# Optimization experiments

Measured on AMD Instinct MI355X. Metric: run time of the kernel, lower is better.

## Reference

```python
import jax, jax.numpy as jnp
import numpy as np

B0, K, H, W = 8, 1, 512, 512
S, CS, NMS, M = 25, 51, 5, 2048
REG_W, COV_POW = 1.0, 0.5

def _gauss_kernel(n):
    x = jnp.linspace(-1.0, 1.0, n)
    g = jnp.exp(-x * x / 0.5)
    return g / g.sum()

def _conv1d2d(x, k1d, horizontal, pad_h, pad_w):
    # x: [B,1,H,W]; replicates torch F.conv2d with the given (possibly asymmetric) padding
    kern = k1d.reshape(1, 1, 1, -1) if horizontal else k1d.reshape(1, 1, -1, 1)
    return jax.lax.conv_general_dilated(x, kern, (1, 1), [(pad_h, pad_h), (pad_w, pad_w)],
                                        dimension_numbers=("NCHW", "OIHW", "NCHW"))

def bilinear_sample(img, pts):
    # img [B,C,H,W], pts [B,N,2] (x,y in [-1,1]); grid_sample bilinear, align_corners=False, zero padding
    Bb, C, Hh, Ww = img.shape
    x = (pts[..., 0] + 1.0) * 0.5 * Ww - 0.5
    y = (pts[..., 1] + 1.0) * 0.5 * Hh - 0.5
    x0 = jnp.floor(x); y0 = jnp.floor(y)
    wx = x - x0; wy = y - y0
    x0i = x0.astype(jnp.int32); y0i = y0.astype(jnp.int32)
    flat = img.reshape(Bb, C, Hh * Ww)
    def tap(yi, xi, w):
        ok = ((yi >= 0) & (yi < Hh) & (xi >= 0) & (xi < Ww)).astype(img.dtype)
        idx = jnp.clip(yi, 0, Hh - 1) * Ww + jnp.clip(xi, 0, Ww - 1)  # [B,N]
        v = jnp.take_along_axis(flat, idx[:, None, :], axis=2)        # [B,C,N]
        return v * (w * ok)[:, None, :]
    return (tap(y0i, x0i, (1 - wy) * (1 - wx)) + tap(y0i, x0i + 1, (1 - wy) * wx)
            + tap(y0i + 1, x0i, wy * (1 - wx)) + tap(y0i + 1, x0i + 1, wy * wx))

def compute_matchability(keypoint_p, has_depth, Bt):
    G = _gauss_kernel(S)
    # NOTE: faithful to original asymmetric padding bug: pad H while convolving along W, then pad W while convolving along H
    s = _conv1d2d(keypoint_p.reshape(Bt, 1, H, W), G, True, S // 2, 0)
    s = _conv1d2d(s, G, False, 0, S // 2)
    log_p_hat = jax.nn.log_softmax(jnp.log(s.reshape(Bt, H * W) + 1e-8), axis=-1)
    sd = _conv1d2d(has_depth.reshape(Bt, 1, H, W), G, True, 0, S // 2)
    sd = _conv1d2d(sd, G, False, S // 2, 0).reshape(Bt, H * W)
    p = sd / sd.sum(-1, keepdims=True)
    return jnp.sum(jnp.where(p > 0, p * (jnp.log(jnp.maximum(p, 1e-30)) - log_p_hat), 0.0), axis=-1)

def sample_keypoints(sm):
    # sm [B,H,W]; coverage-reweighted NMS + top-k (topk=True, subpixel=False)
    wcov = jnp.exp(-jnp.square(jnp.linspace(-2.0, 2.0, CS)))
    ld = _conv1d2d(((sm + 1e-6) * 1e4)[:, None], wcov, True, 0, CS // 2)
    ld = _conv1d2d(ld, wcov, False, CS // 2, 0)[:, 0]
    sm = sm * (ld + 1e-8) ** (-COV_POW)
    p = NMS // 2
    mx = jax.lax.reduce_window(sm, -jnp.inf, jax.lax.max, (1, NMS, NMS), (1, 1, 1),
                               [(0, 0), (p, p), (p, p)])
    sm = sm * (sm == mx)
    _, inds = jax.lax.top_k(sm.reshape(-1, H * W), M)
    xs = (jnp.arange(W) + 0.5) * 2.0 / W - 1.0
    ys = (jnp.arange(H) + 0.5) * 2.0 / H - 1.0
    grid = jnp.stack(jnp.meshgrid(xs, ys, indexing="xy"), axis=-1).reshape(H * W, 2)
    return jnp.take(grid, inds, axis=0)  # [B,M,2] normalized (x,y)

def masked_log_softmax(logits, mask):
    return jax.nn.log_softmax(jnp.where(mask, logits, -1e9), axis=-1)

def _reward(d):
    return jnp.exp(-100.0 * d)

def _forward(scoremap, gt_warp_A2B, gt_warp_B2A, valid_A2B, valid_B2A, has_depth):
    sg = jax.lax.stop_gradient
    lA = scoremap[:B0].reshape(B0, K, H * W)
    lB = scoremap[B0:].reshape(B0, K, H * W)
    logits = jnp.concatenate([lA, lB], 0)                                   # [2B,K,HW]
    kp_p = jax.nn.softmax(logits.reshape(2 * B0, K * H * W), -1).reshape(2 * B0, K, H * W).sum(1)
    match_loss = compute_matchability(kp_p, sg(has_depth), 2 * B0).mean()
    # sparse branch is under torch.set_grad_enabled(False)
    kpts_A = sample_keypoints(sg(kp_p[:B0]).reshape(B0, H, W))
    kpts_B = sample_keypoints(sg(kp_p[B0:]).reshape(B0, H, W))
    kpts_A2B = bilinear_sample(sg(gt_warp_A2B[..., 2:]).transpose(0, 3, 1, 2), kpts_A).transpose(0, 2, 1)
    kpts_B2A = bilinear_sample(sg(gt_warp_B2A[..., 2:]).transpose(0, 3, 1, 2), kpts_B).transpose(0, 2, 1)
    legit_A2B = bilinear_sample(sg(valid_A2B)[:, None], kpts_A)[:, 0] > 0   # [B,M]
    legit_B2A = bilinear_sample(sg(valid_B2A)[:, None], kpts_B)[:, 0] > 0
    dA = jnp.sqrt(jnp.sum(jnp.square(kpts_A2B[:, :, None] - kpts_B[:, None]), -1) + 1e-12).min(-1)
    dB = jnp.sqrt(jnp.sum(jnp.square(kpts_B2A[:, :, None] - kpts_A[:, None]), -1) + 1e-12).min(-1)
    rA = _reward(dA); rB = _reward(dB)
    slA = bilinear_sample(lA.reshape(B0, 1, H, W), kpts_A)[:, 0]            # [B,M]
    slB = bilinear_sample(lB.reshape(B0, 1, H, W), kpts_B)[:, 0]
    lpA = masked_log_softmax(slA, legit_A2B)
    lpB = masked_log_softmax(slB, legit_B2A)
    sparse = -jnp.sum(jnp.where(legit_A2B, rA * lpA, 0.0)) - jnp.sum(jnp.where(legit_B2A, rB * lpB, 0.0))
    return sparse + REG_W * match_loss

def setup_inputs() -> dict:
    key = jax.random.key(0)
    ks = jax.random.split(key, 6)
    scoremap = jax.random.normal(ks[0], (2 * B0, K, H, W), jnp.float32)
    gt_warp_A2B = jax.random.uniform(ks[1], (B0, H, W, 4), jnp.float32, -1.0, 1.0)
    gt_warp_B2A = jax.random.uniform(ks[2], (B0, H, W, 4), jnp.float32, -1.0, 1.0)
    valid_A2B = (jax.random.uniform(ks[3], (B0, H, W)) > 0.3).astype(jnp.float32)
    valid_B2A = (jax.random.uniform(ks[4], (B0, H, W)) > 0.3).astype(jnp.float32)
    has_depth = (jax.random.uniform(ks[5], (2 * B0, H, W)) > 0.3).astype(jnp.float32)
    return dict(scoremap=scoremap, gt_warp_A2B=gt_warp_A2B, gt_warp_B2A=gt_warp_B2A,
                valid_A2B=valid_A2B, valid_B2A=valid_B2A, has_depth=has_depth)

def reference(scoremap, gt_warp_A2B, gt_warp_B2A, valid_A2B, valid_B2A, has_depth):
    return _forward(scoremap, gt_warp_A2B, gt_warp_B2A, valid_A2B, valid_B2A, has_depth)
```

## Files before the change

### kernel.cpp

```cpp
#include <hip/hip_runtime.h>

#define HH 512
#define WW 512
#define HW_ 262144
#define NIMG 16
#define MK 2048
#define CAPB 4096
#define SCAP 32768
#define SBUFN 768

static constexpr size_t OFF_B1    = 16777216;
static constexpr size_t OFF_SMALL = 50331648;
static constexpr size_t OFF_SEL  = 4194304;
static constexpr size_t OFF_BND  = 4325376;
static constexpr size_t OFF_PP   = 4849664;
static constexpr size_t OFF_WXp  = 5111808;
static constexpr size_t OFF_WYp  = 5242880;
static constexpr size_t OFF_LG   = 5373952;
static constexpr size_t OFF_SL   = 5505024;
static constexpr size_t OFF_PMIN = 5636096;
static constexpr size_t OFF_HIST = 33554432;
static constexpr size_t OFF_SURV = 33554432 + 4194304;

#define CSTRIDE 32

__device__ __forceinline__ float wred64(float v) {
  for (int m = 1; m < 64; m <<= 1) v += __shfl_xor(v, m);
  return v;
}

__device__ __forceinline__ void g25_wave0(float* g) {
  int t = threadIdx.x;
  if (t < 64) {
    float raw = 0.0f;
    if (t < 25) {
      float x = -1.0f + (float)t * (2.0f / 24.0f);
      raw = expf(-(x * x) / 0.5f);
    }
    float s = raw;
    for (int m = 1; m < 64; m <<= 1) s += __shfl_xor(s, m);
    if (t < 25) g[t] = raw / s;
  }
}
__device__ __forceinline__ void w51_wave0(float* wc) {
  int t = threadIdx.x;
  if (t < 51) {
    float x = -2.0f + (float)t * (4.0f / 50.0f);
    wc[t] = expf(-x * x);
  }
}

template<int B>
__device__ __forceinline__ float brsum(float v, float* red) {
  int t = threadIdx.x;
  red[t] = v; __syncthreads();
  for (int s = B >> 1; s > 0; s >>= 1) {
    if (t < s) red[t] += red[t + s];
    __syncthreads();
  }
  float r = red[0]; __syncthreads();
  return r;
}
template<int B>
__device__ __forceinline__ float brmax(float v, float* red) {
  int t = threadIdx.x;
  red[t] = v; __syncthreads();
  for (int s = B >> 1; s > 0; s >>= 1) {
    if (t < s) red[t] = fmaxf(red[t], red[t + s]);
    __syncthreads();
  }
  float r = red[0]; __syncthreads();
  return r;
}

__global__ void __launch_bounds__(256)
k_pre(const float* __restrict__ x, const float* __restrict__ hd, float* A,
      float* sume, float* sumS, float* Zb) {
  __shared__ float g[25];
  __shared__ float gp[26];
  __shared__ float red[12];
  int tid = threadIdx.x;
  g25_wave0(g);
  if (tid == 0) {
    float c = 0.0f;
    gp[0] = 0.0f;
    for (int k = 0; k < 25; k++) { c += g[k]; gp[k + 1] = c; }
  }
  size_t base = (size_t)blockIdx.x * 1024;
  size_t e = base + tid * 4;
  float4 xs = *(const float4*)(x + e);
  float4 hs = *(const float4*)(hd + e);
  __syncthreads();
  int rem = (int)(e & (HW_ - 1));
  int y = rem >> 9, x0 = rem & 511;
  float wv;
  {
    int k0 = y - 499; if (k0 < 0) k0 = 0;
    int k1 = y + 12;  if (k1 > 24) k1 = 24;
    wv = gp[k1 + 1] - gp[k0];
  }
  float cwv[4], cpv[4];
#pragma unroll
  for (int q = 0; q < 4; q++) {
    int i = x0 + q;
    int lo = i - 487; if (lo < 0) lo = 0;
    int hi = i;       if (hi > 24) hi = 24;
    cwv[q] = gp[hi + 1] - gp[lo];
    int lo2 = i - 499; if (lo2 < 0) lo2 = 0;
    int hi2 = i + 12;  if (hi2 > 24) hi2 = 24;
    cpv[q] = gp[hi2 + 1] - gp[lo2];
  }
  float e0 = expf(xs.x), e1 = expf(xs.y), e2 = expf(xs.z), e3 = expf(xs.w);
  *(float4*)(A + e) = make_float4(e0, e1, e2, e3);
  float r0 = (e0 + e1) + (e2 + e3);
  float r1 = (e0 * cwv[0] + e1 * cwv[1] + e2 * cwv[2] + e3 * cwv[3]) * wv;
  float r2 = (hs.x * cpv[0] + hs.y * cpv[1] + hs.z * cpv[2] + hs.w * cpv[3]) * wv;
  r0 = wred64(r0); r1 = wred64(r1); r2 = wred64(r2);
  int wid = tid >> 6;
  if ((tid & 63) == 0) { red[wid] = r0; red[4 + wid] = r1; red[8 + wid] = r2; }
  __syncthreads();
  if (tid == 0) {
    int img = (int)(base >> 18);
    atomicAdd(&sume[img * CSTRIDE], red[0] + red[1] + red[2] + red[3]);
    atomicAdd(&sumS[img * CSTRIDE], red[4] + red[5] + red[6] + red[7]);
    atomicAdd(&Zb[img * CSTRIDE], red[8] + red[9] + red[10] + red[11]);
  }
}

__global__ void __launch_bounds__(256)
k_hconv(const float* __restrict__ A, const float* __restrict__ hd,
        const float* __restrict__ sume, float* b12) {
  __shared__ __align__(16) float ta[512];
  __shared__ __align__(16) float th[536];
  __shared__ float g[25];
  int tid = threadIdx.x;
  int blk = blockIdx.x;
  int img = blk >> 9;
  size_t rowoff = (size_t)blk * 512;
  g25_wave0(g);
  ((float2*)ta)[tid] = *(const float2*)(A + rowoff + tid * 2);
  ((float2*)(th + 12))[tid] = *(const float2*)(hd + rowoff + tid * 2);
  if (tid < 12) { th[tid] = 0.0f; th[524 + tid] = 0.0f; }
  __syncthreads();
  float inv = 1.0f / sume[img * CSTRIDE];
  int j = 2 * tid;
  float v1a = 0.0f, v1b = 0.0f;
  if (tid >= 6 && tid <= 249) {
    float w[26];
#pragma unroll
    for (int d = 0; d < 26; d++) w[d] = ta[j - 12 + d];
#pragma unroll
    for (int d = 0; d < 25; d++) {
      v1a = fmaf(g[d], w[d], v1a);
      v1b = fmaf(g[d], w[d + 1], v1b);
    }
  }
  float v2a = 0.0f, v2b = 0.0f;
  {
    float u[26];
#pragma unroll
    for (int d = 0; d < 26; d++) u[d] = th[j + d];
#pragma unroll
    for (int d = 0; d < 25; d++) {
      v2a = fmaf(g[d], u[d], v2a);
      v2b = fmaf(g[d], u[d + 1], v2b);
    }
  }
  *(float4*)(b12 + (rowoff + j) * 2) =
      make_float4(v1a * inv, v2a, v1b * inv, v2b);
}

__global__ void __launch_bounds__(256)
k_match(const float* __restrict__ b12,
        const float* __restrict__ sume, const float* sumS, const float* Zb,
        float* macc) {
  __shared__ float g[25];
  __shared__ __align__(16) float t12[88 * 128];
  __shared__ float red4[4];
  g25_wave0(g);
  int blk = blockIdx.x;
  int img = blk >> 6;
  int ty = (blk >> 3) & 7;
  int tx = blk & 7;
  int y0 = ty * 64, x0 = tx * 64;
  const float* base12 = b12 + (size_t)img * HW_ * 2;
  for (int i = threadIdx.x; i < 88 * 32; i += 256) {
    int r = i >> 5, c4 = i & 31;
    int y = y0 + r - 12;
    float4 v = make_float4(0.f, 0.f, 0.f, 0.f);
    if (y >= 0 && y < 512) {
      size_t px = (size_t)y * 512 + x0 + c4 * 2;
      v = *(const float4*)(base12 + px * 2);
    }
    *(float4*)(t12 + r * 128 + c4 * 4) = v;
  }
  __syncthreads();
  float Z = Zb[img * CSTRIDE];
  float inv = 1.0f / sume[img * CSTRIDE];
  float logS = logf(sumS[img * CSTRIDE] * inv + (float)HW_ * 1e-8f);
  float acc = 0.0f;
  for (int w = threadIdx.x; w < 1024; w += 256) {
    int rg = w >> 6, c = w & 63;
    int r0 = rg * 4;
    float s[4] = {0.f, 0.f, 0.f, 0.f};
    float d[4] = {0.f, 0.f, 0.f, 0.f};
#pragma unroll
    for (int i = 0; i < 28; i++) {
      float2 v = *(const float2*)(t12 + (r0 + i) * 128 + c * 2);
#pragma unroll
      for (int jj = 0; jj < 4; jj++) {
        if (i >= jj && i - jj < 25) {
          s[jj] = fmaf(g[i - jj], v.x, s[jj]);
          d[jj] = fmaf(g[i - jj], v.y, d[jj]);
        }
      }
    }
#pragma unroll
    for (int jj = 0; jj < 4; jj++) {
      float p = d[jj] / Z;
      if (p > 0.0f)
        acc += p * (logf(fmaxf(p, 1e-30f)) - (logf(s[jj] + 1e-8f) - logS));
    }
  }
  acc = wred64(acc);
  if ((threadIdx.x & 63) == 0) red4[threadIdx.x >> 6] = acc;
  __syncthreads();
  if (threadIdx.x == 0)
    atomicAdd(macc, red4[0] + red4[1] + red4[2] + red4[3]);
}

__global__ void __launch_bounds__(256)
k_h51(const float* __restrict__ A, const float* __restrict__ sume, float* out,
      unsigned* __restrict__ hist) {
  __shared__ float wc[51];
  __shared__ __align__(16) float ta[564];
  int tid = threadIdx.x;
  int blk = blockIdx.x;
  int img = blk >> 9;
  size_t rowoff = (size_t)blk * 512;
  w51_wave0(wc);
  if (tid < 32)
    ((uint4*)hist)[(size_t)blk * 32 + tid] = make_uint4(0u, 0u, 0u, 0u);
  float s1 = 1e4f / sume[img * CSTRIDE];
  for (int i = tid; i < 562; i += 256) {
    int j = i - 25;
    ta[i] = ((unsigned)j < 512u) ? fmaf(A[rowoff + j], s1, 1e-2f) : 0.0f;
  }
  __syncthreads();
  int j = 2 * tid;
  float w[52];
#pragma unroll
  for (int d = 0; d < 52; d++) w[d] = ta[j + d];
  float va = 0.0f, vb = 0.0f;
#pragma unroll
  for (int d = 0; d < 51; d++) {
    va = fmaf(wc[d], w[d], va);
    vb = fmaf(wc[d], w[d + 1], vb);
  }
  ((float2*)out)[blk * 256 + tid] = make_float2(va, vb);
}

__global__ void __launch_bounds__(512, 6)
k_smwnms(const float* __restrict__ A, const float* __restrict__ sume,
         const float* __restrict__ b1,
         unsigned long long* surv, unsigned* scnt, unsigned* hist) {
  __shared__ float wc[53];
  __shared__ __align__(16) float tb1[119 * 68];
  __shared__ __align__(16) float tsm[68 * 68];
  __shared__ unsigned lcnt;
  __shared__ unsigned gbase;
  float* hm = tb1;
  unsigned long long* sbuf = (unsigned long long*)(tb1 + 4352);
  int tid = threadIdx.x;
  w51_wave0(wc);
  if (tid == 51 || tid == 52) wc[tid] = 0.0f;
  if (tid == 0) lcnt = 0;
  int blk = blockIdx.x;
  int img = blk >> 6;
  int ty = (blk >> 3) & 7;
  int tx = blk & 7;
  int y0 = ty * 64, x0 = tx * 64;
  const float* base = b1 + (size_t)img * HW_;
  {
    float2 vreg[8];
    int laddr[8];
#pragma unroll
    for (int k = 0; k < 8; k++) {
      int i = tid + k * 512;
      bool ok = (i < 119 * 34);
      int r = i / 34, c2 = i - r * 34;
      int y = y0 + r - 27;
      int x = x0 + c2 * 2 - 2;
      float2 v = make_float2(0.0f, 0.0f);
      if (ok && (unsigned)y < 512u && (unsigned)x < 512u)
        v = *(const float2*)(base + (size_t)y * 512 + x);
      vreg[k] = v;
      laddr[k] = ok ? (r * 68 + c2 * 2) : -1;
    }
#pragma unroll
    for (int k = 0; k < 8; k++)
      if (laddr[k] >= 0) *(float2*)(tb1 + laddr[k]) = vreg[k];
  }
  __syncthreads();
  float inv = 1.0f / sume[img * CSTRIDE];
  const float* abase = A + (size_t)img * HW_;
  if (tid < 23 * 17) {
    int rg = tid / 17, cg = tid - rg * 17;
    int r0 = rg * 3, c0 = cg * 4;
    int nr = (r0 <= 65) ? 3 : 2;
    float2 apre[3][2];
#pragma unroll
    for (int jj = 0; jj < 3; jj++) {
      int y = y0 + r0 + jj - 2;
      int xb = x0 + c0 - 2;
      apre[jj][0] = make_float2(0.f, 0.f);
      apre[jj][1] = make_float2(0.f, 0.f);
      if ((unsigned)y < 512u) {
        const float* ar = abase + (size_t)y * 512;
        if ((unsigned)xb < 512u) apre[jj][0] = *(const float2*)(ar + xb);
        if ((unsigned)(xb + 2) < 512u) apre[jj][1] = *(const float2*)(ar + xb + 2);
      }
    }
    float a0x = 0.f, a0y = 0.f, a0z = 0.f, a0w = 0.f;
    float a1x = 0.f, a1y = 0.f, a1z = 0.f, a1w = 0.f;
    float a2x = 0.f, a2y = 0.f, a2z = 0.f, a2w = 0.f;
    float w1 = 0.f, w2 = 0.f;
    const float* tp = tb1 + r0 * 68 + c0;
#pragma unroll 4
    for (int i = 0; i < 53; i++) {
      float4 v = *(const float4*)(tp + i * 68);
      float w0 = wc[i];
      a0x = fmaf(w0, v.x, a0x); a0y = fmaf(w0, v.y, a0y);
      a0z = fmaf(w0, v.z, a0z); a0w = fmaf(w0, v.w, a0w);
      a1x = fmaf(w1, v.x, a1x); a1y = fmaf(w1, v.y, a1y);
      a1z = fmaf(w1, v.z, a1z); a1w = fmaf(w1, v.w, a1w);
      a2x = fmaf(w2, v.x, a2x); a2y = fmaf(w2, v.y, a2y);
      a2z = fmaf(w2, v.z, a2z); a2w = fmaf(w2, v.w, a2w);
      w2 = w1; w1 = w0;
    }
    auto storerow = [&](int jj, float ax, float ay, float az, float aw,
                        float2 p0, float2 p1) {
      int r = r0 + jj;
      int y = y0 + r - 2;
      int xb = x0 + c0 - 2;
      float4 res = make_float4(-3.4e38f, -3.4e38f, -3.4e38f, -3.4e38f);
      if ((unsigned)y < 512u) {
        if ((unsigned)xb < 512u) {
          res.x = (p0.x * inv) / sqrtf(ax + 1e-8f);
          res.y = (p0.y * inv) / sqrtf(ay + 1e-8f);
        }
        if ((unsigned)(xb + 2) < 512u) {
          res.z = (p1.x * inv) / sqrtf(az + 1e-8f);
          res.w = (p1.y * inv) / sqrtf(aw + 1e-8f);
        }
      }
      *(float4*)(tsm + r * 68 + c0) = res;
    };
    storerow(0, a0x, a0y, a0z, a0w, apre[0][0], apre[0][1]);
    storerow(1, a1x, a1y, a1z, a1w, apre[1][0], apre[1][1]);
    if (nr == 3) storerow(2, a2x, a2y, a2z, a2w, apre[2][0], apre[2][1]);
  }
  __syncthreads();
  for (int i = tid; i < 68 * 16; i += 512) {
    int r = i >> 4, cg = i & 15;
    const float* row = tsm + r * 68 + cg * 4;
    float4 v0 = *(const float4*)(row);
    float4 v1 = *(const float4*)(row + 4);
    float p01 = fmaxf(v0.x, v0.y), p12 = fmaxf(v0.y, v0.z);
    float p23 = fmaxf(v0.z, v0.w), p34 = fmaxf(v0.w, v1.x);
    float p45 = fmaxf(v1.x, v1.y), p56 = fmaxf(v1.y, v1.z);
    float m0 = fmaxf(fmaxf(p01, p23), v1.x);
    float m1 = fmaxf(fmaxf(p12, p34), v1.y);
    float m2 = fmaxf(fmaxf(p23, p45), v1.z);
    float m3 = fmaxf(fmaxf(p34, p56), v1.w);
    *(float4*)(hm + r * 64 + cg * 4) = make_float4(m0, m1, m2, m3);
  }
  __syncthreads();
  for (int k0 = 0; k0 < 2; k0++) {
    int i = tid + k0 * 512;
    int r = i >> 4, cb = (i & 15) * 4;
    const float* tp2 = tsm + (r + 2) * 68 + cb + 2;
    float2 va = *(const float2*)(tp2);
    float2 vb = *(const float2*)(tp2 + 2);
    float4 m0 = *(const float4*)(hm + r * 64 + cb);
    float4 m1 = *(const float4*)(hm + (r + 1) * 64 + cb);
    float4 m2 = *(const float4*)(hm + (r + 2) * 64 + cb);
    float4 m3 = *(const float4*)(hm + (r + 3) * 64 + cb);
    float4 m4 = *(const float4*)(hm + (r + 4) * 64 + cb);
    float Mx = fmaxf(fmaxf(m0.x, m1.x), fmaxf(fmaxf(m2.x, m3.x), m4.x));
    float My = fmaxf(fmaxf(m0.y, m1.y), fmaxf(fmaxf(m2.y, m3.y), m4.y));
    float Mz = fmaxf(fmaxf(m0.z, m1.z), fmaxf(fmaxf(m2.z, m3.z), m4.z));
    float Mw = fmaxf(fmaxf(m0.w, m1.w), fmaxf(fmaxf(m2.w, m3.w), m4.w));
    auto keepf = [&](float vk, float Mk, int k) {
      if (vk == Mk && vk != 0.0f) {
        unsigned p = atomicAdd(&lcnt, 1u);
        unsigned bits = __float_as_uint(vk);
        unsigned idx = (unsigned)((y0 + r) * 512 + x0 + cb + k);
        if (p < SBUFN)
          sbuf[p] = ((unsigned long long)bits << 32) |
                    (unsigned long long)(idx ^ 0xFFFFFFFFu);
        atomicAdd(&hist[(size_t)img * 65536 + (bits >> 16)], 1u);
      }
    };
    keepf(va.x, Mx, 0); keepf(va.y, My, 1);
    keepf(vb.x, Mz, 2); keepf(vb.y, Mw, 3);
  }
  __syncthreads();
  unsigned total = lcnt; if (total > SBUFN) total = SBUFN;
  if (tid == 0) gbase = atomicAdd(&scnt[img * CSTRIDE], total);
  __syncthreads();
  unsigned gb = gbase;
  for (unsigned i = tid; i < total; i += 512) {
    unsigned p = gb + i;
    if (p < SCAP) surv[(size_t)img * SCAP + p] = sbuf[i];
  }
}

__global__ void __launch_bounds__(1024)
k_thresh(const unsigned* __restrict__ hist, unsigned* Tb, unsigned* needb) {
  int img = blockIdx.x;
  const unsigned* h = hist + (size_t)img * 65536;
  __shared__ unsigned wsum[16];
  __shared__ unsigned wpre[16];
  int t = threadIdx.x;
  int b0 = 65472 - 64 * t;
  const uint4* hv = (const uint4*)(h + b0);
  unsigned s = 0;
#pragma unroll
  for (int k = 0; k < 16; k++) {
    uint4 u = hv[k];
    s += u.x + u.y + u.z + u.w;
  }
  if (b0 == 0) s += 0x00100000u - h[0];
  unsigned inc = s;
  for (int m = 1; m < 64; m <<= 1) {
    unsigned o = __shfl_up(inc, m);
    if ((t & 63) >= m) inc += o;
  }
  if ((t & 63) == 63) wsum[t >> 6] = inc;
  __syncthreads();
  if (t < 16) {
    unsigned p = 0;
    for (int k = 0; k < 16; k++) if (k < t) p += wsum[k];
    wpre[t] = p;
  }
  __syncthreads();
  unsigned pre = wpre[t >> 6] + inc - s;
  if (pre < MK && pre + s >= MK) {
    unsigned c = pre;
    for (int k = 0; k < 64; k++) {
      int bin = 65535 - (t * 64 + k);
      unsigned cnt = (bin == 0) ? 0x00100000u : h[bin];
      if (c + cnt >= MK) { Tb[img * CSTRIDE] = (unsigned)bin; needb[img * CSTRIDE] = MK - c; break; }
      c += cnt;
    }
  }
}

__global__ void k_collect(const unsigned long long* __restrict__ surv,
                          const unsigned* __restrict__ scnt,
                          const unsigned* __restrict__ Tb,
                          unsigned* selcnt, unsigned* sel,
                          unsigned* bcnt, unsigned long long* bnd) {
  int blk = blockIdx.x;
  int img = blk >> 7;
  int i = (blk & 127) * 256 + threadIdx.x;
  unsigned cnt = scnt[img * CSTRIDE]; if (cnt > SCAP) cnt = SCAP;
  unsigned long long entry = ((unsigned)i < cnt) ? surv[(size_t)img * SCAP + i] : 0ull;
  unsigned bits = (unsigned)(entry >> 32);
  unsigned bin = bits >> 16;
  unsigned T = Tb[img * CSTRIDE];
  bool ok = (unsigned)i < cnt;
  bool c1 = ok && (bin > T);
  bool c2 = ok && (bin == T);
  int lane = threadIdx.x & 63;
  unsigned long long lowmask = (1ull << lane) - 1ull;

  unsigned long long m1 = __ballot(c1);
  if (m1) {
    int leader = __ffsll(m1) - 1;
    unsigned base = 0;
    if (lane == leader) base = atomicAdd(&selcnt[img * CSTRIDE], (unsigned)__popcll(m1));
    base = __shfl(base, leader);
    if (c1) {
      unsigned p = base + (unsigned)__popcll(m1 & lowmask);
      if (p < MK) sel[img * MK + p] = (unsigned)(entry & 0xFFFFFFFFull) ^ 0xFFFFFFFFu;
    }
  }
  unsigned long long m2 = __ballot(c2);
  if (m2) {
    int leader = __ffsll(m2) - 1;
    unsigned base = 0;
    if (lane == leader) base = atomicAdd(&bcnt[img * CSTRIDE], (unsigned)__popcll(m2));
    base = __shfl(base, leader);
    if (c2) {
      unsigned p = base + (unsigned)__popcll(m2 & lowmask);
      if (p < CAPB) bnd[(size_t)img * CAPB + p] = entry;
    }
  }
}

__global__ void __launch_bounds__(1024)
k_finsel(const unsigned long long* __restrict__ bnd, const unsigned* bcnt,
         const unsigned* needb, const unsigned* selcnt, unsigned* sel) {
  int img = blockIdx.x;
  __shared__ unsigned long long key[CAPB];
  unsigned bn = bcnt[img * CSTRIDE];
  int n = (bn < CAPB) ? (int)bn : CAPB;
  int np2 = 2;
  while (np2 < n) np2 <<= 1;
  int t = threadIdx.x;
  for (int k = t; k < np2; k += 1024)
    key[k] = (k < n) ? bnd[(size_t)img * CAPB + k] : 0ull;
  __syncthreads();
  for (int sz = 2; sz <= np2; sz <<= 1) {
    for (int st = sz >> 1; st > 0; st >>= 1) {
      for (int i = t; i < np2; i += 1024) {
        int l = i ^ st;
        if (l > i) {
          unsigned long long a = key[i], b = key[l];
          bool up = ((i & sz) == 0);
          if (up ? (a < b) : (a > b)) { key[i] = b; key[l] = a; }
        }
      }
      __syncthreads();
    }
  }
  unsigned c1 = selcnt[img * CSTRIDE]; if (c1 > MK) c1 = MK;
  unsigned need = needb[img * CSTRIDE];
  unsigned kk = need; if (kk > MK - c1) kk = MK - c1;
  for (unsigned m = t; m < MK - c1; m += 1024) {
    unsigned v = 0u;
    if (m < kk && m < (unsigned)n)
      v = (unsigned)(key[m] & 0xFFFFFFFFull) ^ 0xFFFFFFFFu;
    sel[img * MK + c1 + m] = v;
  }
}

__global__ void k_prep(const unsigned* __restrict__ sel, const float* __restrict__ scoremap,
                       const float* __restrict__ gtA, const float* __restrict__ gtB,
                       const float* __restrict__ vA, const float* __restrict__ vB,
                       float2* pp, float* wx, float* wy, float* lg, float* sl) {
  int t = blockIdx.x * 256 + threadIdx.x;
  int img = t >> 11;
  unsigned idx = sel[t] & (HW_ - 1);
  int h = idx >> 9, w = idx & 511;
  pp[t] = make_float2((w + 0.5f) * (2.0f / 512.0f) - 1.0f,
                      (h + 0.5f) * (2.0f / 512.0f) - 1.0f);
  int b = (img < 8) ? img : img - 8;
  const float* gt = (img < 8) ? gtA : gtB;
  const float* vv = (img < 8) ? vA : vB;
  size_t pix = (size_t)b * HW_ + idx;
  float2 gxy = *(const float2*)(gt + pix * 4 + 2);
  wx[t] = gxy.x;
  wy[t] = gxy.y;
  lg[t] = (vv[pix] > 0.0f) ? 1.0f : 0.0f;
  sl[t] = scoremap[(size_t)img * HW_ + idx];
}

__global__ void __launch_bounds__(256)
k_mindist(const float2* __restrict__ pp,
          const float* __restrict__ wx, const float* __restrict__ wy,
          float* pmin) {
  __shared__ float2 opp[512];
  int blk = blockIdx.x;
  int img = blk >> 5;
  int qc = (blk >> 2) & 7;
  int oc = blk & 3;
  const float2* ob = pp + (size_t)(img ^ 8) * MK + oc * 512;
  for (int k = threadIdx.x; k < 512; k += 256) opp[k] = ob[k];
  __syncthreads();
  int m = img * MK + qc * 256 + threadIdx.x;
  float ax = wx[m], ay = wy[m];
  float d[8];
#pragma unroll
  for (int u = 0; u < 8; u++) d[u] = 3.4e38f;
  for (int n = 0; n < 512; n += 8) {
#pragma unroll
    for (int u = 0; u < 8; u++) {
      float2 o = opp[n + u];
      float dx = ax - o.x, dy = ay - o.y;
      d[u] = fminf(d[u], fmaf(dx, dx, dy * dy));
    }
  }
  float d2 = fminf(fminf(fminf(d[0], d[1]), fminf(d[2], d[3])),
                   fminf(fminf(d[4], d[5]), fminf(d[6], d[7])));
  pmin[oc * (NIMG * MK) + m] = d2;
}

__global__ void __launch_bounds__(1024)
k_loss(const float* __restrict__ sl, const float* __restrict__ lg,
       const float* __restrict__ pmin, float* sacc, float* macc, float* out,
       unsigned* ldone) {
  int img = blockIdx.x;
  __shared__ float red[1024];
  int t = threadIdx.x;
  int i0 = img * MK + t, i1 = i0 + 1024;
  float s0 = sl[i0], s1 = sl[i1];
  float g0 = lg[i0], g1 = lg[i1];
  float l0 = (g0 > 0.0f) ? s0 : -1e9f;
  float l1 = (g1 > 0.0f) ? s1 : -1e9f;
  float mx = brmax<1024>(fmaxf(l0, l1), red);
  float se = brsum<1024>(expf(l0 - mx) + expf(l1 - mx), red);
  float lse = mx + logf(se);
  const int ST = NIMG * MK;
  float a = 0.0f;
  if (g0 > 0.0f) {
    float mn = fminf(fminf(pmin[i0], pmin[ST + i0]),
                     fminf(pmin[2 * ST + i0], pmin[3 * ST + i0]));
    float r0 = expf(-100.0f * sqrtf(mn + 1e-12f));
    a += r0 * (s0 - lse);
  }
  if (g1 > 0.0f) {
    float mn = fminf(fminf(pmin[i1], pmin[ST + i1]),
                     fminf(pmin[2 * ST + i1], pmin[3 * ST + i1]));
    float r1 = expf(-100.0f * sqrtf(mn + 1e-12f));
    a += r1 * (s1 - lse);
  }
  float tot = brsum<1024>(a, red);
  if (t == 0) {
    atomicAdd(sacc, -tot);
    __threadfence();
    unsigned dnum = atomicAdd(ldone, 1u);
    if (dnum == NIMG - 1) {
      float sv = atomicAdd(sacc, 0.0f);
      float mv = atomicAdd(macc, 0.0f);
      out[0] = sv + mv * (1.0f / 16.0f);
    }
  }
}

extern "C" void kernel_launch(void* const* d_in, const int* in_sizes, int n_in,
                              void* d_out, int out_size, void* d_ws, size_t ws_size,
                              hipStream_t stream) {
  const float* scoremap = (const float*)d_in[0];
  const float* gtA = (const float*)d_in[1];
  const float* gtB = (const float*)d_in[2];
  const float* vA  = (const float*)d_in[3];
  const float* vB  = (const float*)d_in[4];
  const float* hd  = (const float*)d_in[5];

  char* ws = (char*)d_ws;
  float* A   = (float*)(ws);
  float* B12 = (float*)(ws + OFF_B1);
  float* B1p = (float*)(ws + OFF_B1);

  char* sm = ws + OFF_SMALL;
  float*    sume   = (float*)(sm + 0);
  float*    sumS   = (float*)(sm + 2048);
  float*    Zb     = (float*)(sm + 4096);
  unsigned* Tb     = (unsigned*)(sm + 6144);
  unsigned* needb  = (unsigned*)(sm + 8192);
  unsigned* selcnt = (unsigned*)(sm + 10240);
  unsigned* bcnt   = (unsigned*)(sm + 12288);
  float*    macc   = (float*)(sm + 14336);
  float*    sacc   = (float*)(sm + 14464);
  unsigned* scnt   = (unsigned*)(sm + 16384);
  unsigned* ldone  = (unsigned*)(sm + 20480);

  unsigned* hist = (unsigned*)(ws + OFF_HIST);
  unsigned long long* surv = (unsigned long long*)(ws + OFF_SURV);
  unsigned* sel  = (unsigned*)(ws + OFF_SEL);
  unsigned long long* bnd = (unsigned long long*)(ws + OFF_BND);
  float2* pp = (float2*)(ws + OFF_PP);
  float* wx = (float*)(ws + OFF_WXp);
  float* wy = (float*)(ws + OFF_WYp);
  float* lg = (float*)(ws + OFF_LG);
  float* sl = (float*)(ws + OFF_SL);
  float* pmin = (float*)(ws + OFF_PMIN);

  float* out = (float*)d_out;

  hipMemsetAsync(sm, 0, 32768, stream);

  k_pre<<<4096, 256, 0, stream>>>(scoremap, hd, A, sume, sumS, Zb);

  k_hconv<<<8192, 256, 0, stream>>>(A, hd, sume, B12);
  k_match<<<1024, 256, 0, stream>>>(B12, sume, sumS, Zb, macc);

  k_h51<<<8192, 256, 0, stream>>>(A, sume, B1p, hist);

  k_smwnms<<<1024, 512, 0, stream>>>(A, sume, B1p, surv, scnt, hist);
  k_thresh<<<16, 1024, 0, stream>>>(hist, Tb, needb);
  k_collect<<<2048, 256, 0, stream>>>(surv, scnt, Tb, selcnt, sel, bcnt, bnd);
  k_finsel<<<16, 1024, 0, stream>>>(bnd, bcnt, needb, selcnt, sel);

  k_prep<<<128, 256, 0, stream>>>(sel, scoremap, gtA, gtB, vA, vB, pp, wx, wy, lg, sl);
  k_mindist<<<512, 256, 0, stream>>>(pp, wx, wy, pmin);
  k_loss<<<16, 1024, 0, stream>>>(sl, lg, pmin, sacc, macc, out, ldone);
}
```

Baseline: 288.5 us.

## Stream vertical convolutions from global memory into register sliding windows

Both k_match and k_smwnms stop staging halo tiles in shared memory. Each thread now walks down one column straight from global memory and accumulates 16 or 17 output rows in registers using a shifting weight window. k_smwnms also folds the horizontal and vertical max passes into a single 5x5 pass read from the tsm tile, and its launch bounds go from 6 to 8 blocks. The goal is to cut LDS traffic and footprint and raise occupancy, at the cost of strided uncoalesced-per-thread global loads, higher register pressure, and threads idling on the 68-of-128 column mapping.

After: 660.4 us. 2.29x slower.

```diff
diff --git a/kernel.cpp b/kernel.cpp
--- a/kernel.cpp
+++ b/kernel.cpp
@@ -174,58 +174,57 @@
 k_match(const float* __restrict__ b12,
         const float* __restrict__ sume, const float* sumS, const float* Zb,
         float* macc) {
-  __shared__ float g[25];
-  __shared__ __align__(16) float t12[88 * 128];
+  __shared__ float g[40];
   __shared__ float red4[4];
+  int tid = threadIdx.x;
   g25_wave0(g);
+  if (tid >= 25 && tid < 40) g[tid] = 0.0f;
   int blk = blockIdx.x;
   int img = blk >> 6;
   int ty = (blk >> 3) & 7;
   int tx = blk & 7;
   int y0 = ty * 64, x0 = tx * 64;
   const float* base12 = b12 + (size_t)img * HW_ * 2;
-  for (int i = threadIdx.x; i < 88 * 32; i += 256) {
-    int r = i >> 5, c4 = i & 31;
-    int y = y0 + r - 12;
-    float4 v = make_float4(0.f, 0.f, 0.f, 0.f);
-    if (y >= 0 && y < 512) {
-      size_t px = (size_t)y * 512 + x0 + c4 * 2;
-      v = *(const float4*)(base12 + px * 2);
-    }
-    *(float4*)(t12 + r * 128 + c4 * 4) = v;
-  }
-  __syncthreads();
   float Z = Zb[img * CSTRIDE];
-  float inv = 1.0f / sume[img * CSTRIDE];
-  float logS = logf(sumS[img * CSTRIDE] * inv + (float)HW_ * 1e-8f);
+  float invs = 1.0f / sume[img * CSTRIDE];
+  float logS = logf(sumS[img * CSTRIDE] * invs + (float)HW_ * 1e-8f);
+  __syncthreads();
+  int seg = tid >> 6;
+  int c = tid & 63;
+  int r0 = seg * 16;
+  const float* colp = base12 + (size_t)(x0 + c) * 2;
+  float s[16], d[16], wreg[16];
+#pragma unroll
+  for (int jj = 0; jj < 16; jj++) { s[jj] = 0.f; d[jj] = 0.f; wreg[jj] = 0.f; }
+  int ybase = y0 + r0 - 12;
+#pragma unroll
+  for (int i = 0; i < 40; i++) {
+    int y = ybase + i;
+    float vx = 0.0f, vy = 0.0f;
+    if ((unsigned)y < 512u) {
+      float2 v = *(const float2*)(colp + (size_t)y * 1024);
+      vx = v.x; vy = v.y;
+    }
+#pragma unroll
+    for (int jj = 15; jj >= 1; jj--) wreg[jj] = wreg[jj - 1];
+    wreg[0] = g[i];
+#pragma unroll
+    for (int jj = 0; jj < 16; jj++) {
+      s[jj] = fmaf(wreg[jj], vx, s[jj]);
+      d[jj] = fmaf(wreg[jj], vy, d[jj]);
+    }
+  }
   float acc = 0.0f;
-  for (int w = threadIdx.x; w < 1024; w += 256) {
-    int rg = w >> 6, c = w & 63;
-    int r0 = rg * 4;
-    float s[4] = {0.f, 0.f, 0.f, 0.f};
-    float d[4] = {0.f, 0.f, 0.f, 0.f};
-#pragma unroll
-    for (int i = 0; i < 28; i++) {
-      float2 v = *(const float2*)(t12 + (r0 + i) * 128 + c * 2);
-#pragma unroll
-      for (int jj = 0; jj < 4; jj++) {
-        if (i >= jj && i - jj < 25) {
-          s[jj] = fmaf(g[i - jj], v.x, s[jj]);
-          d[jj] = fmaf(g[i - jj], v.y, d[jj]);
-        }
-      }
-    }
-#pragma unroll
-    for (int jj = 0; jj < 4; jj++) {
-      float p = d[jj] / Z;
-      if (p > 0.0f)
-        acc += p * (logf(fmaxf(p, 1e-30f)) - (logf(s[jj] + 1e-8f) - logS));
-    }
+#pragma unroll
+  for (int jj = 0; jj < 16; jj++) {
+    float p = d[jj] / Z;
+    if (p > 0.0f)
+      acc += p * (logf(fmaxf(p, 1e-30f)) - (logf(s[jj] + 1e-8f) - logS));
   }
   acc = wred64(acc);
-  if ((threadIdx.x & 63) == 0) red4[threadIdx.x >> 6] = acc;
-  __syncthreads();
-  if (threadIdx.x == 0)
+  if ((tid & 63) == 0) red4[tid >> 6] = acc;
+  __syncthreads();
+  if (tid == 0)
     atomicAdd(macc, red4[0] + red4[1] + red4[2] + red4[3]);
 }
 
@@ -260,20 +259,18 @@
   ((float2*)out)[blk * 256 + tid] = make_float2(va, vb);
 }
 
-__global__ void __launch_bounds__(512, 6)
+__global__ void __launch_bounds__(512, 8)
 k_smwnms(const float* __restrict__ A, const float* __restrict__ sume,
          const float* __restrict__ b1,
          unsigned long long* surv, unsigned* scnt, unsigned* hist) {
-  __shared__ float wc[53];
-  __shared__ __align__(16) float tb1[119 * 68];
+  __shared__ float wc[68];
   __shared__ __align__(16) float tsm[68 * 68];
+  __shared__ unsigned long long sbuf[SBUFN];
   __shared__ unsigned lcnt;
   __shared__ unsigned gbase;
-  float* hm = tb1;
-  unsigned long long* sbuf = (unsigned long long*)(tb1 + 4352);
   int tid = threadIdx.x;
   w51_wave0(wc);
-  if (tid == 51 || tid == 52) wc[tid] = 0.0f;
+  if (tid >= 51 && tid < 68) wc[tid] = 0.0f;
   if (tid == 0) lcnt = 0;
   int blk = blockIdx.x;
   int img = blk >> 6;
@@ -281,116 +278,72 @@
   int tx = blk & 7;
   int y0 = ty * 64, x0 = tx * 64;
   const float* base = b1 + (size_t)img * HW_;
-  {
-    float2 vreg[8];
-    int laddr[8];
-#pragma unroll
-    for (int k = 0; k < 8; k++) {
-      int i = tid + k * 512;
-      bool ok = (i < 119 * 34);
-      int r = i / 34, c2 = i - r * 34;
-      int y = y0 + r - 27;
-      int x = x0 + c2 * 2 - 2;
-      float2 v = make_float2(0.0f, 0.0f);
-      if (ok && (unsigned)y < 512u && (unsigned)x < 512u)
-        v = *(const float2*)(base + (size_t)y * 512 + x);
-      vreg[k] = v;
-      laddr[k] = ok ? (r * 68 + c2 * 2) : -1;
-    }
-#pragma unroll
-    for (int k = 0; k < 8; k++)
-      if (laddr[k] >= 0) *(float2*)(tb1 + laddr[k]) = vreg[k];
-  }
-  __syncthreads();
+  const float* abase = A + (size_t)img * HW_;
   float inv = 1.0f / sume[img * CSTRIDE];
-  const float* abase = A + (size_t)img * HW_;
-  if (tid < 23 * 17) {
-    int rg = tid / 17, cg = tid - rg * 17;
-    int r0 = rg * 3, c0 = cg * 4;
-    int nr = (r0 <= 65) ? 3 : 2;
-    float2 apre[3][2];
-#pragma unroll
-    for (int jj = 0; jj < 3; jj++) {
+  __syncthreads();
+  int seg = tid >> 7;
+  int c = tid & 127;
+  if (c < 68) {
+    int r0 = seg * 17;
+    int x = x0 + c - 2;
+    bool xok = (unsigned)x < 512u;
+    int xc = xok ? x : 0;
+    const float* colp = base + xc;
+    float acc[17], wreg[17];
+#pragma unroll
+    for (int jj = 0; jj < 17; jj++) { acc[jj] = 0.0f; wreg[jj] = 0.0f; }
+    int ybase = y0 + r0 - 27;
+#pragma unroll
+    for (int i = 0; i < 67; i++) {
+      int y = ybase + i;
+      float v = 0.0f;
+      if ((unsigned)y < 512u) {
+        v = colp[(size_t)y * 512];
+        if (!xok) v = 0.0f;
+      }
+#pragma unroll
+      for (int jj = 16; jj >= 1; jj--) wreg[jj] = wreg[jj - 1];
+      wreg[0] = wc[i];
+#pragma unroll
+      for (int jj = 0; jj < 17; jj++) acc[jj] = fmaf(wreg[jj], v, acc[jj]);
+    }
+#pragma unroll
+    for (int jj = 0; jj < 17; jj++) acc[jj] = inv / sqrtf(acc[jj] + 1e-8f);
+#pragma unroll
+    for (int jj = 0; jj < 17; jj++) {
       int y = y0 + r0 + jj - 2;
-      int xb = x0 + c0 - 2;
-      apre[jj][0] = make_float2(0.f, 0.f);
-      apre[jj][1] = make_float2(0.f, 0.f);
-      if ((unsigned)y < 512u) {
-        const float* ar = abase + (size_t)y * 512;
-        if ((unsigned)xb < 512u) apre[jj][0] = *(const float2*)(ar + xb);
-        if ((unsigned)(xb + 2) < 512u) apre[jj][1] = *(const float2*)(ar + xb + 2);
-      }
-    }
-    float a0x = 0.f, a0y = 0.f, a0z = 0.f, a0w = 0.f;
-    float a1x = 0.f, a1y = 0.f, a1z = 0.f, a1w = 0.f;
-    float a2x = 0.f, a2y = 0.f, a2z = 0.f, a2w = 0.f;
-    float w1 = 0.f, w2 = 0.f;
-    const float* tp = tb1 + r0 * 68 + c0;
-#pragma unroll 4
-    for (int i = 0; i < 53; i++) {
-      float4 v = *(const float4*)(tp + i * 68);
-      float w0 = wc[i];
-      a0x = fmaf(w0, v.x, a0x); a0y = fmaf(w0, v.y, a0y);
-      a0z = fmaf(w0, v.z, a0z); a0w = fmaf(w0, v.w, a0w);
-      a1x = fmaf(w1, v.x, a1x); a1y = fmaf(w1, v.y, a1y);
-      a1z = fmaf(w1, v.z, a1z); a1w = fmaf(w1, v.w, a1w);
-      a2x = fmaf(w2, v.x, a2x); a2y = fmaf(w2, v.y, a2y);
-      a2z = fmaf(w2, v.z, a2z); a2w = fmaf(w2, v.w, a2w);
-      w2 = w1; w1 = w0;
-    }
-    auto storerow = [&](int jj, float ax, float ay, float az, float aw,
-                        float2 p0, float2 p1) {
-      int r = r0 + jj;
-      int y = y0 + r - 2;
-      int xb = x0 + c0 - 2;
-      float4 res = make_float4(-3.4e38f, -3.4e38f, -3.4e38f, -3.4e38f);
-      if ((unsigned)y < 512u) {
-        if ((unsigned)xb < 512u) {
-          res.x = (p0.x * inv) / sqrtf(ax + 1e-8f);
-          res.y = (p0.y * inv) / sqrtf(ay + 1e-8f);
-        }
-        if ((unsigned)(xb + 2) < 512u) {
-          res.z = (p1.x * inv) / sqrtf(az + 1e-8f);
-          res.w = (p1.y * inv) / sqrtf(aw + 1e-8f);
-        }
-      }
-      *(float4*)(tsm + r * 68 + c0) = res;
-    };
-    storerow(0, a0x, a0y, a0z, a0w, apre[0][0], apre[0][1]);
-    storerow(1, a1x, a1y, a1z, a1w, apre[1][0], apre[1][1]);
-    if (nr == 3) storerow(2, a2x, a2y, a2z, a2w, apre[2][0], apre[2][1]);
-  }
-  __syncthreads();
-  for (int i = tid; i < 68 * 16; i += 512) {
-    int r = i >> 4, cg = i & 15;
-    const float* row = tsm + r * 68 + cg * 4;
-    float4 v0 = *(const float4*)(row);
-    float4 v1 = *(const float4*)(row + 4);
-    float p01 = fmaxf(v0.x, v0.y), p12 = fmaxf(v0.y, v0.z);
-    float p23 = fmaxf(v0.z, v0.w), p34 = fmaxf(v0.w, v1.x);
-    float p45 = fmaxf(v1.x, v1.y), p56 = fmaxf(v1.y, v1.z);
-    float m0 = fmaxf(fmaxf(p01, p23), v1.x);
-    float m1 = fmaxf(fmaxf(p12, p34), v1.y);
-    float m2 = fmaxf(fmaxf(p23, p45), v1.z);
-    float m3 = fmaxf(fmaxf(p34, p56), v1.w);
-    *(float4*)(hm + r * 64 + cg * 4) = make_float4(m0, m1, m2, m3);
+      float res = -3.4e38f;
+      if ((unsigned)y < 512u && xok)
+        res = abase[(size_t)y * 512 + xc] * acc[jj];
+      tsm[(r0 + jj) * 68 + c] = res;
+    }
   }
   __syncthreads();
   for (int k0 = 0; k0 < 2; k0++) {
     int i = tid + k0 * 512;
     int r = i >> 4, cb = (i & 15) * 4;
-    const float* tp2 = tsm + (r + 2) * 68 + cb + 2;
-    float2 va = *(const float2*)(tp2);
-    float2 vb = *(const float2*)(tp2 + 2);
-    float4 m0 = *(const float4*)(hm + r * 64 + cb);
-    float4 m1 = *(const float4*)(hm + (r + 1) * 64 + cb);
-    float4 m2 = *(const float4*)(hm + (r + 2) * 64 + cb);
-    float4 m3 = *(const float4*)(hm + (r + 3) * 64 + cb);
-    float4 m4 = *(const float4*)(hm + (r + 4) * 64 + cb);
-    float Mx = fmaxf(fmaxf(m0.x, m1.x), fmaxf(fmaxf(m2.x, m3.x), m4.x));
-    float My = fmaxf(fmaxf(m0.y, m1.y), fmaxf(fmaxf(m2.y, m3.y), m4.y));
-    float Mz = fmaxf(fmaxf(m0.z, m1.z), fmaxf(fmaxf(m2.z, m3.z), m4.z));
-    float Mw = fmaxf(fmaxf(m0.w, m1.w), fmaxf(fmaxf(m2.w, m3.w), m4.w));
+    const float* t0 = tsm + r * 68 + cb;
+    float4 ra[5], rb[5];
+#pragma unroll
+    for (int k = 0; k < 5; k++) {
+      ra[k] = *(const float4*)(t0 + k * 68);
+      rb[k] = *(const float4*)(t0 + k * 68 + 4);
+    }
+    float Mx = -3.4e38f, My = -3.4e38f, Mz = -3.4e38f, Mw = -3.4e38f;
+#pragma unroll
+    for (int k = 0; k < 5; k++) {
+      float4 a = ra[k], b = rb[k];
+      float pyz = fmaxf(a.y, a.z);
+      float pzw = fmaxf(a.z, a.w);
+      float pwb = fmaxf(a.w, b.x);
+      float pbx = fmaxf(b.x, b.y);
+      float pby = fmaxf(b.y, b.z);
+      Mx = fmaxf(Mx, fmaxf(fmaxf(a.x, pyz), pwb));
+      My = fmaxf(My, fmaxf(fmaxf(pyz, pwb), b.y));
+      Mz = fmaxf(Mz, fmaxf(fmaxf(pzw, pbx), b.z));
+      Mw = fmaxf(Mw, fmaxf(fmaxf(pwb, pby), b.w));
+    }
+    float vx = ra[2].z, vy = ra[2].w, vz = rb[2].x, vw = rb[2].y;
     auto keepf = [&](float vk, float Mk, int k) {
       if (vk == Mk && vk != 0.0f) {
         unsigned p = atomicAdd(&lcnt, 1u);
@@ -402,8 +355,8 @@
         atomicAdd(&hist[(size_t)img * 65536 + (bits >> 16)], 1u);
       }
     };
-    keepf(va.x, Mx, 0); keepf(va.y, My, 1);
-    keepf(vb.x, Mz, 2); keepf(vb.y, Mw, 3);
+    keepf(vx, Mx, 0); keepf(vy, My, 1);
+    keepf(vz, Mz, 2); keepf(vw, Mw, 3);
   }
   __syncthreads();
   unsigned total = lcnt; if (total > SBUFN) total = SBUFN;
```

## Stream columns from global memory with register sliding window in k_match

Applied to the files above, without the earlier changes.

Removes the 88x128 shared-memory tile in k_match. Each thread now reads its own column straight from global memory and computes 16 vertical outputs with a shifting register window of Gaussian weights, replacing 4-output groups over LDS. This drops the LDS staging, its barrier and the repeated shared reads. In exchange it uses more registers and makes strided, uncoalesced-per-row global loads, reading 40 rows per 16 outputs instead of 28 per 4.

Result: no change. 287.0 us, median of 3 (-0.5%).

```diff
diff --git a/kernel.cpp b/kernel.cpp
--- a/kernel.cpp
+++ b/kernel.cpp
@@ -174,58 +174,57 @@
 k_match(const float* __restrict__ b12,
         const float* __restrict__ sume, const float* sumS, const float* Zb,
         float* macc) {
-  __shared__ float g[25];
-  __shared__ __align__(16) float t12[88 * 128];
+  __shared__ float g[40];
   __shared__ float red4[4];
+  int tid = threadIdx.x;
   g25_wave0(g);
+  if (tid >= 25 && tid < 40) g[tid] = 0.0f;
   int blk = blockIdx.x;
   int img = blk >> 6;
   int ty = (blk >> 3) & 7;
   int tx = blk & 7;
   int y0 = ty * 64, x0 = tx * 64;
   const float* base12 = b12 + (size_t)img * HW_ * 2;
-  for (int i = threadIdx.x; i < 88 * 32; i += 256) {
-    int r = i >> 5, c4 = i & 31;
-    int y = y0 + r - 12;
-    float4 v = make_float4(0.f, 0.f, 0.f, 0.f);
-    if (y >= 0 && y < 512) {
-      size_t px = (size_t)y * 512 + x0 + c4 * 2;
-      v = *(const float4*)(base12 + px * 2);
-    }
-    *(float4*)(t12 + r * 128 + c4 * 4) = v;
-  }
-  __syncthreads();
   float Z = Zb[img * CSTRIDE];
-  float inv = 1.0f / sume[img * CSTRIDE];
-  float logS = logf(sumS[img * CSTRIDE] * inv + (float)HW_ * 1e-8f);
+  float invs = 1.0f / sume[img * CSTRIDE];
+  float logS = logf(sumS[img * CSTRIDE] * invs + (float)HW_ * 1e-8f);
+  __syncthreads();
+  int seg = tid >> 6;
+  int c = tid & 63;
+  int r0 = seg * 16;
+  const float* colp = base12 + (size_t)(x0 + c) * 2;
+  float s[16], d[16], wreg[16];
+#pragma unroll
+  for (int jj = 0; jj < 16; jj++) { s[jj] = 0.f; d[jj] = 0.f; wreg[jj] = 0.f; }
+  int ybase = y0 + r0 - 12;
+#pragma unroll
+  for (int i = 0; i < 40; i++) {
+    int y = ybase + i;
+    float vx = 0.0f, vy = 0.0f;
+    if ((unsigned)y < 512u) {
+      float2 v = *(const float2*)(colp + (size_t)y * 1024);
+      vx = v.x; vy = v.y;
+    }
+#pragma unroll
+    for (int jj = 15; jj >= 1; jj--) wreg[jj] = wreg[jj - 1];
+    wreg[0] = g[i];
+#pragma unroll
+    for (int jj = 0; jj < 16; jj++) {
+      s[jj] = fmaf(wreg[jj], vx, s[jj]);
+      d[jj] = fmaf(wreg[jj], vy, d[jj]);
+    }
+  }
   float acc = 0.0f;
-  for (int w = threadIdx.x; w < 1024; w += 256) {
-    int rg = w >> 6, c = w & 63;
-    int r0 = rg * 4;
-    float s[4] = {0.f, 0.f, 0.f, 0.f};
-    float d[4] = {0.f, 0.f, 0.f, 0.f};
-#pragma unroll
-    for (int i = 0; i < 28; i++) {
-      float2 v = *(const float2*)(t12 + (r0 + i) * 128 + c * 2);
-#pragma unroll
-      for (int jj = 0; jj < 4; jj++) {
-        if (i >= jj && i - jj < 25) {
-          s[jj] = fmaf(g[i - jj], v.x, s[jj]);
-          d[jj] = fmaf(g[i - jj], v.y, d[jj]);
-        }
-      }
-    }
-#pragma unroll
-    for (int jj = 0; jj < 4; jj++) {
-      float p = d[jj] / Z;
-      if (p > 0.0f)
-        acc += p * (logf(fmaxf(p, 1e-30f)) - (logf(s[jj] + 1e-8f) - logS));
-    }
+#pragma unroll
+  for (int jj = 0; jj < 16; jj++) {
+    float p = d[jj] / Z;
+    if (p > 0.0f)
+      acc += p * (logf(fmaxf(p, 1e-30f)) - (logf(s[jj] + 1e-8f) - logS));
   }
   acc = wred64(acc);
-  if ((threadIdx.x & 63) == 0) red4[threadIdx.x >> 6] = acc;
-  __syncthreads();
-  if (threadIdx.x == 0)
+  if ((tid & 63) == 0) red4[tid >> 6] = acc;
+  __syncthreads();
+  if (tid == 0)
     atomicAdd(macc, red4[0] + red4[1] + red4[2] + red4[3]);
 }
 
```
